# Optimization experiments

Measured on AMD Instinct MI355X. Metric: run time of the kernel, lower is better.

Reference implementation:

```python
import jax, jax.numpy as jnp
import numpy as np

LN_EPS = 1e-5
IH_IDX = np.array([0, 2, 4, 6])  # layernorm_iih, fih, aih, oih
HH_IDX = np.array([1, 3, 5, 7])  # layernorm_ihh, fhh, ahh, ohh


def _ln(x, g, b):
    # LayerNorm over last dim, matching nn.LayerNorm(hidden_size)
    mu = jnp.mean(x, axis=-1, keepdims=True)
    xc = x - mu
    var = jnp.mean(xc * xc, axis=-1, keepdims=True)
    return g * xc * jax.lax.rsqrt(var + LN_EPS) + b


def setup_inputs() -> dict:
    B, I, H = 4096, 1024, 1024
    key = jax.random.key(0)
    ks = jax.random.split(key, 8)
    stdv = 1.0 / np.sqrt(H)  # reset_parameters: uniform(-stdv, stdv)
    return {
        "x": jax.random.normal(ks[0], (B, I), jnp.float32),
        "h": jax.random.normal(ks[1], (B, H), jnp.float32),
        "c": jax.random.normal(ks[2], (B, H), jnp.float32),
        "w_ih": jax.random.uniform(ks[3], (4 * H, I), jnp.float32, -stdv, stdv),
        "w_hh": jax.random.uniform(ks[4], (4 * H, H), jnp.float32, -stdv, stdv),
        "b_ih": jax.random.uniform(ks[5], (4 * H,), jnp.float32, -stdv, stdv),
        # 9 LayerNorms stacked: [iih, ihh, fih, fhh, aih, ahh, oih, ohh, ct]
        "ln_gamma": 1.0 + 0.1 * jax.random.normal(ks[6], (9, H), jnp.float32),
        "ln_beta": 0.1 * jax.random.normal(ks[7], (9, H), jnp.float32),
        "time": 0,
    }


def reference(x, h, c, w_ih, w_hh, b_ih, ln_gamma, ln_beta, time):
    B = x.shape[0]
    H = w_hh.shape[1]
    # pre-activations, split into the 4 gates (i, f, a, o) along dim 1
    pre_ih = (x @ w_ih.T).reshape(B, 4, H)   # [B,4,H]
    pre_hh = (h @ w_hh.T).reshape(B, 4, H)   # [B,4,H]
    # per-gate LayerNorm on ih and hh contributions, then add bias
    gates = (
        _ln(pre_ih, ln_gamma[IH_IDX], ln_beta[IH_IDX])
        + _ln(pre_hh, ln_gamma[HH_IDX], ln_beta[HH_IDX])
        + b_ih.reshape(4, H)
    )
    i, f, a, o = gates[:, 0], gates[:, 1], gates[:, 2], gates[:, 3]
    c_new = jax.nn.sigmoid(f) * c + jax.nn.sigmoid(i) * jnp.tanh(a)
    h_new = jax.nn.sigmoid(o) * jnp.tanh(_ln(c_new, ln_gamma[8], ln_beta[8]))
    return (h_new, c_new)
```

## Files before the change

kernel.cpp:

```cpp
#include <hip/hip_runtime.h>
#include <hip/hip_bf16.h>
#include <stdint.h>


#define HDIM 1024
#define BATCH 4096
#define NGATE 4096
#define KDIM 1024

typedef __bf16 bf16x8 __attribute__((ext_vector_type(8)));
typedef float f32x4 __attribute__((ext_vector_type(4)));
typedef unsigned short ushort8_t __attribute__((ext_vector_type(8)));

__device__ __forceinline__ unsigned short f2bf(float f) {
  unsigned int u = __builtin_bit_cast(unsigned int, f);
  unsigned int r = (u + 0x7fffu + ((u >> 16) & 1u)) >> 16;
  return (unsigned short)r;
}

__device__ __forceinline__ float bf2f(unsigned short s) {
  unsigned int u = ((unsigned int)s) << 16;
  return __builtin_bit_cast(float, u);
}

__device__ __forceinline__ void gl_lds16(const void* g, void* l) {
  __builtin_amdgcn_global_load_lds(
      (__attribute__((address_space(1))) unsigned int*)g,
      (__attribute__((address_space(3))) unsigned int*)l,
      16, 0, 0);
}

__global__ __launch_bounds__(256) void cast_bf16_kernel(
    const float* __restrict__ x, const float* __restrict__ h,
    const float* __restrict__ wi, const float* __restrict__ wh,
    unsigned short* __restrict__ xb, unsigned short* __restrict__ hb,
    unsigned short* __restrict__ wib, unsigned short* __restrict__ whb) {
  const float* src;
  unsigned short* dst;
  switch (blockIdx.y) {
    case 0: src = x;  dst = xb;  break;
    case 1: src = h;  dst = hb;  break;
    case 2: src = wi; dst = wib; break;
    default: src = wh; dst = whb; break;
  }
  size_t i = ((size_t)blockIdx.x * 256 + threadIdx.x) * 4;
  float4 v = *(const float4*)(src + i);
  ushort4 o;
  o.x = f2bf(v.x); o.y = f2bf(v.y); o.z = f2bf(v.z); o.w = f2bf(v.w);
  *(ushort4*)(dst + i) = o;
}

__global__ __launch_bounds__(256, 4) void gemm_bt_kernel(
    const unsigned short* __restrict__ A0, const unsigned short* __restrict__ B0,
    unsigned short* __restrict__ C0,
    const unsigned short* __restrict__ A1, const unsigned short* __restrict__ B1,
    unsigned short* __restrict__ C1) {
  const unsigned short* A = blockIdx.z ? A1 : A0;
  const unsigned short* B = blockIdx.z ? B1 : B0;
  unsigned short* C = blockIdx.z ? C1 : C0;

  __shared__ alignas(16) unsigned short As[128 * 64];
  __shared__ alignas(16) unsigned short Bs[128 * 64];

  const int tid = threadIdx.x;
  const int wave = tid >> 6;
  const int lane = tid & 63;
  const int bm = blockIdx.x * 128;
  const int bn = blockIdx.y * 128;
  const int wm = (wave >> 1) * 64;
  const int wn = (wave & 1) * 64;

  const int srow = lane >> 3;
  const int scol = (((lane & 7) ^ (lane >> 3)) * 8);

  f32x4 acc[4][4];
#pragma unroll
  for (int i = 0; i < 4; ++i)
#pragma unroll
    for (int j = 0; j < 4; ++j)
#pragma unroll
      for (int r = 0; r < 4; ++r) acc[i][j][r] = 0.0f;

  const int m15 = lane & 15;
  const int quad = lane >> 4;

  for (int k0 = 0; k0 < KDIM; k0 += 64) {
#pragma unroll
    for (int t = 0; t < 4; ++t) {
      int R = wave * 32 + t * 8;
      gl_lds16(A + (size_t)(bm + R + srow) * KDIM + k0 + scol, &As[R * 64]);
      gl_lds16(B + (size_t)(bn + R + srow) * KDIM + k0 + scol, &Bs[R * 64]);
    }
    __syncthreads();

#pragma unroll
    for (int s = 0; s < 2; ++s) {
      bf16x8 af[4], bfr[4];
#pragma unroll
      for (int i = 0; i < 4; ++i) {
        int row = wm + i * 16 + m15;
        af[i] = *(const bf16x8*)&As[row * 64 + (((4 * s + quad) ^ (m15 & 7)) * 8)];
      }
#pragma unroll
      for (int j = 0; j < 4; ++j) {
        int row = wn + j * 16 + m15;
        bfr[j] = *(const bf16x8*)&Bs[row * 64 + (((4 * s + quad) ^ (m15 & 7)) * 8)];
      }
#pragma unroll
      for (int i = 0; i < 4; ++i)
#pragma unroll
        for (int j = 0; j < 4; ++j)
          acc[i][j] = __builtin_amdgcn_mfma_f32_16x16x32_bf16(af[i], bfr[j], acc[i][j], 0, 0, 0);
    }

    __syncthreads();
  }

#pragma unroll
  for (int i = 0; i < 4; ++i)
#pragma unroll
    for (int j = 0; j < 4; ++j)
#pragma unroll
      for (int r = 0; r < 4; ++r) {
        int m = bm + wm + i * 16 + quad * 4 + r;
        int n = bn + wn + j * 16 + m15;
        C[(size_t)m * NGATE + n] = f2bf(acc[i][j][r]);
      }
}

__device__ __forceinline__ float fast_sigmoid(float x) {
  return __builtin_amdgcn_rcpf(1.0f + __expf(-x));
}
__device__ __forceinline__ float fast_tanh(float x) {
  return 1.0f - 2.0f * __builtin_amdgcn_rcpf(__expf(2.0f * x) + 1.0f);
}

__global__ __launch_bounds__(256) void ln_gate_kernel(
    const unsigned short* __restrict__ pih, const unsigned short* __restrict__ phh,
    const float* __restrict__ c, const float* __restrict__ b_ih,
    const float* __restrict__ gamma, const float* __restrict__ beta,
    float* __restrict__ h_out, float* __restrict__ c_out) {
  __shared__ float lds[32];
  const int b = blockIdx.x;
  const int t = threadIdx.x;
  const int wave = t >> 6;
  const int lane = t & 63;
  const float inv_h = 1.0f / 1024.0f;
  const float eps = 1e-5f;

  {
    const size_t rb = (size_t)b * NGATE + wave * HDIM + lane * 16;
    ushort8_t a0 = *(const ushort8_t*)&pih[rb];
    ushort8_t a1 = *(const ushort8_t*)&pih[rb + 8];
    ushort8_t e0 = *(const ushort8_t*)&phh[rb];
    ushort8_t e1 = *(const ushort8_t*)&phh[rb + 8];
    float s0 = 0.f, q0 = 0.f, s1 = 0.f, q1 = 0.f;
#pragma unroll
    for (int r = 0; r < 8; ++r) {
      float va = bf2f(a0[r]), vb = bf2f(a1[r]);
      float ea = bf2f(e0[r]), eb = bf2f(e1[r]);
      s0 += va + vb; q0 += va * va + vb * vb;
      s1 += ea + eb; q1 += ea * ea + eb * eb;
    }
#pragma unroll
    for (int o = 1; o < 64; o <<= 1) {
      s0 += __shfl_xor(s0, o, 64); q0 += __shfl_xor(q0, o, 64);
      s1 += __shfl_xor(s1, o, 64); q1 += __shfl_xor(q1, o, 64);
    }
    if (lane == 0) {
      float mu0 = s0 * inv_h;
      float mu1 = s1 * inv_h;
      lds[wave * 4 + 0] = mu0;
      lds[wave * 4 + 1] = rsqrtf(q0 * inv_h - mu0 * mu0 + eps);
      lds[wave * 4 + 2] = mu1;
      lds[wave * 4 + 3] = rsqrtf(q1 * inv_h - mu1 * mu1 + eps);
    }
  }
  __syncthreads();

  const int j = t * 4;
  float gate[4][4];
#pragma unroll
  for (int g = 0; g < 4; ++g) {
    float mu0 = lds[g * 4 + 0], rs0 = lds[g * 4 + 1];
    float mu1 = lds[g * 4 + 2], rs1 = lds[g * 4 + 3];
    ushort4 a4 = *(const ushort4*)&pih[(size_t)b * NGATE + g * HDIM + j];
    ushort4 e4 = *(const ushort4*)&phh[(size_t)b * NGATE + g * HDIM + j];
    float vih[4] = {bf2f(a4.x), bf2f(a4.y), bf2f(a4.z), bf2f(a4.w)};
    float vhh[4] = {bf2f(e4.x), bf2f(e4.y), bf2f(e4.z), bf2f(e4.w)};
    float4 g0 = *(const float4*)&gamma[(2 * g) * HDIM + j];
    float4 b0 = *(const float4*)&beta[(2 * g) * HDIM + j];
    float4 g1 = *(const float4*)&gamma[(2 * g + 1) * HDIM + j];
    float4 b1 = *(const float4*)&beta[(2 * g + 1) * HDIM + j];
    float4 bb = *(const float4*)&b_ih[g * HDIM + j];
    const float* g0p = &g0.x; const float* b0p = &b0.x;
    const float* g1p = &g1.x; const float* b1p = &b1.x;
    const float* bbp = &bb.x;
#pragma unroll
    for (int r = 0; r < 4; ++r) {
      float gih = g0p[r] * ((vih[r] - mu0) * rs0) + b0p[r];
      float ghh = g1p[r] * ((vhh[r] - mu1) * rs1) + b1p[r];
      gate[g][r] = gih + ghh + bbp[r];
    }
  }

  float4 cv4 = *(const float4*)&c[(size_t)b * HDIM + j];
  const float* cvp = &cv4.x;
  float cn[4], ov[4];
  float s2 = 0.f, q2 = 0.f;
#pragma unroll
  for (int r = 0; r < 4; ++r) {
    float iv = fast_sigmoid(gate[0][r]);
    float fv = fast_sigmoid(gate[1][r]);
    float av = fast_tanh(gate[2][r]);
    ov[r] = fast_sigmoid(gate[3][r]);
    float cvn = fv * cvp[r] + iv * av;
    cn[r] = cvn;
    s2 += cvn; q2 += cvn * cvn;
  }
#pragma unroll
  for (int o = 1; o < 64; o <<= 1) {
    s2 += __shfl_xor(s2, o, 64);
    q2 += __shfl_xor(q2, o, 64);
  }
  __syncthreads();
  if (lane == 0) { lds[16 + wave * 2] = s2; lds[16 + wave * 2 + 1] = q2; }
  __syncthreads();
  s2 = lds[16] + lds[18] + lds[20] + lds[22];
  q2 = lds[17] + lds[19] + lds[21] + lds[23];
  float mu = s2 * inv_h;
  float rs = rsqrtf(q2 * inv_h - mu * mu + eps);

  float4 g8 = *(const float4*)&gamma[8 * HDIM + j];
  float4 b8 = *(const float4*)&beta[8 * HDIM + j];
  const float* g8p = &g8.x; const float* b8p = &b8.x;
  float4 ho, co;
  float* hop = &ho.x; float* cop = &co.x;
#pragma unroll
  for (int r = 0; r < 4; ++r) {
    float ln = g8p[r] * ((cn[r] - mu) * rs) + b8p[r];
    hop[r] = ov[r] * fast_tanh(ln);
    cop[r] = cn[r];
  }
  *(float4*)&h_out[(size_t)b * HDIM + j] = ho;
  *(float4*)&c_out[(size_t)b * HDIM + j] = co;
}

extern "C" void kernel_launch(void* const* d_in, const int* in_sizes, int n_in,
                              void* d_out, int out_size, void* d_ws, size_t ws_size,
                              hipStream_t stream) {
  const float* x     = (const float*)d_in[0];
  const float* h     = (const float*)d_in[1];
  const float* c     = (const float*)d_in[2];
  const float* w_ih  = (const float*)d_in[3];
  const float* w_hh  = (const float*)d_in[4];
  const float* b_ih  = (const float*)d_in[5];
  const float* gamma = (const float*)d_in[6];
  const float* beta  = (const float*)d_in[7];

  char* ws = (char*)d_ws;
  unsigned short* xb  = (unsigned short*)(ws);
  unsigned short* hb  = (unsigned short*)(ws + (size_t)8 * 1024 * 1024);
  unsigned short* wib = (unsigned short*)(ws + (size_t)16 * 1024 * 1024);
  unsigned short* whb = (unsigned short*)(ws + (size_t)24 * 1024 * 1024);
  unsigned short* pih = (unsigned short*)(ws + (size_t)32 * 1024 * 1024);
  unsigned short* phh = (unsigned short*)(ws + (size_t)64 * 1024 * 1024);

  dim3 cgrid(4096, 4, 1);
  cast_bf16_kernel<<<cgrid, 256, 0, stream>>>(x, h, w_ih, w_hh, xb, hb, wib, whb);

  dim3 ggrid(32, 32, 2);
  gemm_bt_kernel<<<ggrid, 256, 0, stream>>>(xb, wib, pih, hb, whb, phh);

  float* h_out = (float*)d_out;
  float* c_out = h_out + (size_t)BATCH * HDIM;
  ln_gate_kernel<<<4096, 256, 0, stream>>>(pih, phh, c, b_ih, gamma, beta, h_out, c_out);
}
```

Baseline: 231.8 us.

## Enlarge GEMM tile to 256x128 and fuse LayerNorm row statistics into epilogue

The GEMM block tile grows from 128x128 to 256x128, with each wave computing 128x64 using 32 accumulators, and launch bounds drop to 2 blocks per SM. The GEMM epilogue now computes per-row partial sums and sums of squares from the fp32 accumulators and writes them to a stats buffer. The LN kernel then reduces these partials instead of re-reading the full bf16 pre-activations to compute its statistics. The larger tile adds register pressure and lowers occupancy, and the statistics now come from fp32 values rather than bf16-rounded ones.

After: 245.0 us. 5.7% more time.

```diff
diff --git a/kernel.cpp b/kernel.cpp
--- a/kernel.cpp
+++ b/kernel.cpp
@@ -50,32 +50,33 @@
   *(ushort4*)(dst + i) = o;
 }
 
-__global__ __launch_bounds__(256, 4) void gemm_bt_kernel(
+__global__ __launch_bounds__(256, 2) void gemm_bt_kernel(
     const unsigned short* __restrict__ A0, const unsigned short* __restrict__ B0,
-    unsigned short* __restrict__ C0,
+    unsigned short* __restrict__ C0, float2* __restrict__ S0,
     const unsigned short* __restrict__ A1, const unsigned short* __restrict__ B1,
-    unsigned short* __restrict__ C1) {
+    unsigned short* __restrict__ C1, float2* __restrict__ S1) {
   const unsigned short* A = blockIdx.z ? A1 : A0;
   const unsigned short* B = blockIdx.z ? B1 : B0;
   unsigned short* C = blockIdx.z ? C1 : C0;
-
-  __shared__ alignas(16) unsigned short As[128 * 64];
+  float2* SB = blockIdx.z ? S1 : S0;
+
+  __shared__ alignas(16) unsigned short As[256 * 64];
   __shared__ alignas(16) unsigned short Bs[128 * 64];
 
   const int tid = threadIdx.x;
   const int wave = tid >> 6;
   const int lane = tid & 63;
-  const int bm = blockIdx.x * 128;
+  const int bm = blockIdx.x * 256;
   const int bn = blockIdx.y * 128;
-  const int wm = (wave >> 1) * 64;
-  const int wn = (wave & 1) * 64;
+  const int wrow = (wave >> 1) * 128;
+  const int wcol = (wave & 1) * 64;
 
   const int srow = lane >> 3;
   const int scol = (((lane & 7) ^ (lane >> 3)) * 8);
 
-  f32x4 acc[4][4];
-#pragma unroll
-  for (int i = 0; i < 4; ++i)
+  f32x4 acc[8][4];
+#pragma unroll
+  for (int i = 0; i < 8; ++i)
 #pragma unroll
     for (int j = 0; j < 4; ++j)
 #pragma unroll
@@ -86,28 +87,30 @@
 
   for (int k0 = 0; k0 < KDIM; k0 += 64) {
 #pragma unroll
+    for (int t = 0; t < 8; ++t) {
+      int R = wave * 64 + t * 8;
+      gl_lds16(A + (size_t)(bm + R + srow) * KDIM + k0 + scol, &As[R * 64]);
+    }
+#pragma unroll
     for (int t = 0; t < 4; ++t) {
       int R = wave * 32 + t * 8;
-      gl_lds16(A + (size_t)(bm + R + srow) * KDIM + k0 + scol, &As[R * 64]);
       gl_lds16(B + (size_t)(bn + R + srow) * KDIM + k0 + scol, &Bs[R * 64]);
     }
     __syncthreads();
 
 #pragma unroll
     for (int s = 0; s < 2; ++s) {
-      bf16x8 af[4], bfr[4];
-#pragma unroll
-      for (int i = 0; i < 4; ++i) {
-        int row = wm + i * 16 + m15;
-        af[i] = *(const bf16x8*)&As[row * 64 + (((4 * s + quad) ^ (m15 & 7)) * 8)];
-      }
-#pragma unroll
-      for (int j = 0; j < 4; ++j) {
-        int row = wn + j * 16 + m15;
-        bfr[j] = *(const bf16x8*)&Bs[row * 64 + (((4 * s + quad) ^ (m15 & 7)) * 8)];
-      }
-#pragma unroll
-      for (int i = 0; i < 4; ++i)
+      const int gran = (((4 * s + quad) ^ (m15 & 7)) * 8);
+      bf16x8 af[8], bfr[4];
+#pragma unroll
+      for (int i = 0; i < 8; ++i)
+        af[i] = *(const bf16x8*)&As[(wrow + i * 16 + m15) * 64 + gran];
+#pragma unroll
+      for (int j = 0; j < 4; ++j)
+        bfr[j] = *(const bf16x8*)&Bs[(wcol + j * 16 + m15) * 64 + gran];
+
+#pragma unroll
+      for (int i = 0; i < 8; ++i)
 #pragma unroll
         for (int j = 0; j < 4; ++j)
           acc[i][j] = __builtin_amdgcn_mfma_f32_16x16x32_bf16(af[i], bfr[j], acc[i][j], 0, 0, 0);
@@ -117,15 +120,36 @@
   }
 
 #pragma unroll
-  for (int i = 0; i < 4; ++i)
+  for (int i = 0; i < 8; ++i)
 #pragma unroll
     for (int j = 0; j < 4; ++j)
 #pragma unroll
       for (int r = 0; r < 4; ++r) {
-        int m = bm + wm + i * 16 + quad * 4 + r;
-        int n = bn + wn + j * 16 + m15;
+        int m = bm + wrow + i * 16 + quad * 4 + r;
+        int n = bn + wcol + j * 16 + m15;
         C[(size_t)m * NGATE + n] = f2bf(acc[i][j][r]);
       }
+
+#pragma unroll
+  for (int i = 0; i < 8; ++i)
+#pragma unroll
+    for (int r = 0; r < 4; ++r) {
+      float s = 0.f, q = 0.f;
+#pragma unroll
+      for (int j = 0; j < 4; ++j) {
+        float v = acc[i][j][r];
+        s += v; q += v * v;
+      }
+#pragma unroll
+      for (int o = 1; o < 16; o <<= 1) {
+        s += __shfl_xor(s, o, 64);
+        q += __shfl_xor(q, o, 64);
+      }
+      if (m15 == 0) {
+        int m = bm + wrow + i * 16 + quad * 4 + r;
+        SB[(size_t)m * 64 + blockIdx.y * 2 + (wave & 1)] = make_float2(s, q);
+      }
+    }
 }
 
 __device__ __forceinline__ float fast_sigmoid(float x) {
@@ -137,6 +161,7 @@
 
 __global__ __launch_bounds__(256) void ln_gate_kernel(
     const unsigned short* __restrict__ pih, const unsigned short* __restrict__ phh,
+    const float2* __restrict__ S0, const float2* __restrict__ S1,
     const float* __restrict__ c, const float* __restrict__ b_ih,
     const float* __restrict__ gamma, const float* __restrict__ beta,
     float* __restrict__ h_out, float* __restrict__ c_out) {
@@ -148,32 +173,20 @@
   const float inv_h = 1.0f / 1024.0f;
   const float eps = 1e-5f;
 
-  {
-    const size_t rb = (size_t)b * NGATE + wave * HDIM + lane * 16;
-    ushort8_t a0 = *(const ushort8_t*)&pih[rb];
-    ushort8_t a1 = *(const ushort8_t*)&pih[rb + 8];
-    ushort8_t e0 = *(const ushort8_t*)&phh[rb];
-    ushort8_t e1 = *(const ushort8_t*)&phh[rb + 8];
-    float s0 = 0.f, q0 = 0.f, s1 = 0.f, q1 = 0.f;
-#pragma unroll
-    for (int r = 0; r < 8; ++r) {
-      float va = bf2f(a0[r]), vb = bf2f(a1[r]);
-      float ea = bf2f(e0[r]), eb = bf2f(e1[r]);
-      s0 += va + vb; q0 += va * va + vb * vb;
-      s1 += ea + eb; q1 += ea * ea + eb * eb;
-    }
-#pragma unroll
-    for (int o = 1; o < 64; o <<= 1) {
-      s0 += __shfl_xor(s0, o, 64); q0 += __shfl_xor(q0, o, 64);
-      s1 += __shfl_xor(s1, o, 64); q1 += __shfl_xor(q1, o, 64);
-    }
-    if (lane == 0) {
-      float mu0 = s0 * inv_h;
-      float mu1 = s1 * inv_h;
-      lds[wave * 4 + 0] = mu0;
-      lds[wave * 4 + 1] = rsqrtf(q0 * inv_h - mu0 * mu0 + eps);
-      lds[wave * 4 + 2] = mu1;
-      lds[wave * 4 + 3] = rsqrtf(q1 * inv_h - mu1 * mu1 + eps);
+  if (t < 128) {
+    const float2* S = wave ? S1 : S0;
+    float2 p = S[(size_t)b * 64 + lane];
+    float s = p.x, q = p.y;
+#pragma unroll
+    for (int o = 1; o < 16; o <<= 1) {
+      s += __shfl_xor(s, o, 64);
+      q += __shfl_xor(q, o, 64);
+    }
+    if ((lane & 15) == 0) {
+      int g = lane >> 4;
+      float mu = s * inv_h;
+      lds[g * 4 + wave * 2 + 0] = mu;
+      lds[g * 4 + wave * 2 + 1] = rsqrtf(q * inv_h - mu * mu + eps);
     }
   }
   __syncthreads();
@@ -265,14 +278,16 @@
   unsigned short* whb = (unsigned short*)(ws + (size_t)24 * 1024 * 1024);
   unsigned short* pih = (unsigned short*)(ws + (size_t)32 * 1024 * 1024);
   unsigned short* phh = (unsigned short*)(ws + (size_t)64 * 1024 * 1024);
+  float2* stat0 = (float2*)(ws + (size_t)96 * 1024 * 1024);
+  float2* stat1 = (float2*)(ws + (size_t)98 * 1024 * 1024);
 
   dim3 cgrid(4096, 4, 1);
   cast_bf16_kernel<<<cgrid, 256, 0, stream>>>(x, h, w_ih, w_hh, xb, hb, wib, whb);
 
-  dim3 ggrid(32, 32, 2);
-  gemm_bt_kernel<<<ggrid, 256, 0, stream>>>(xb, wib, pih, hb, whb, phh);
+  dim3 ggrid(16, 32, 2);
+  gemm_bt_kernel<<<ggrid, 256, 0, stream>>>(xb, wib, pih, stat0, hb, whb, phh, stat1);
 
   float* h_out = (float*)d_out;
   float* c_out = h_out + (size_t)BATCH * HDIM;
-  ln_gate_kernel<<<4096, 256, 0, stream>>>(pih, phh, c, b_ih, gamma, beta, h_out, c_out);
-}
+  ln_gate_kernel<<<4096, 256, 0, stream>>>(pih, phh, stat0, stat1, c, b_ih, gamma, beta, h_out, c_out);
+}
```
